# Optimization experiments

Measured on AMD Instinct MI355X. Metric: run time of the kernel, lower is better.

Reference implementation:

```python
import jax, jax.numpy as jnp
import numpy as np

B, L, D = 8, 2048, 512
H, P = 8, 4
C = D // H  # dim_per_head


def setup_inputs() -> dict:
    key = jax.random.key(0)
    ks = jax.random.split(key, 11)
    sc = lambda k, shape, s=0.02: jax.random.normal(k, shape, jnp.float32) * s
    return dict(
        query=jax.random.normal(ks[0], (B, L, D), jnp.float32),
        key_in=jax.random.normal(ks[1], (B, L, D), jnp.float32),
        value=jax.random.normal(ks[2], (B, L, D), jnp.float32),
        W_v=sc(ks[3], (D, D)), b_v=jnp.zeros((D,), jnp.float32),
        W_off=sc(ks[4], (D, H * P * 2), 0.01), b_off=sc(ks[5], (H * P * 2,), 0.2),
        W_aw=sc(ks[6], (D, H * P), 0.01), b_aw=jnp.zeros((H * P,), jnp.float32),
        W_out=sc(ks[7], (D, D)), b_out=jnp.zeros((D,), jnp.float32),
    )


def reference(query, key_in, value, W_v, b_v, W_off, b_off, W_aw, b_aw, W_out, b_out):
    # value projection
    v = value @ W_v + b_v                                        # (B,L,D)
    # sampling offsets and attention weights from the query
    off = (query @ W_off + b_off).reshape(B, L, H, P, 2)         # (B,L,H,P,2)
    aw = jax.nn.softmax((query @ W_aw + b_aw).reshape(B, L, H, P), axis=-1)
    # reference point for query i is (x=linspace[0]=0, y=linspace[i]) because
    # the torch code slices reference_points[:, :, :, :1, :]
    ref_y = jnp.linspace(0.0, 1.0, L, dtype=jnp.float32)
    loc_x = jnp.clip(off[..., 0], 0.0, 1.0)                      # ref_x = 0
    loc_y = jnp.clip(off[..., 1] + ref_y[None, :, None, None], 0.0, 1.0)
    # grid_sample, align_corners=False, input (BH, C, 1, L)
    ix = ((loc_x + 1.0) * L - 1.0) * 0.5                         # width coord in [ (L-1)/2, L-0.5 ]
    iy = loc_y * 0.5                                             # ((y+1)*1 - 1)/2
    ix0 = jnp.floor(ix)
    fx = ix - ix0
    iy0 = jnp.floor(iy)
    fy = iy - iy0
    # height dim has size 1: row iy0 valid iff ==0, row iy0+1 valid iff ==0 (zero padding)
    ywt = (1.0 - fy) * (iy0 == 0.0).astype(jnp.float32) + fy * ((iy0 + 1.0) == 0.0).astype(jnp.float32)
    i0 = ix0.astype(jnp.int32)
    i1 = i0 + 1

    perm = lambda a: a.transpose(0, 2, 1, 3)                     # (B,L,H,P) -> (B,H,L,P)
    i0p, i1p = perm(i0), perm(i1)
    vh = v.reshape(B, L, H, C).transpose(0, 2, 1, 3)             # (B,H,L,C)

    gather = jax.vmap(jax.vmap(lambda vm, ii: vm[ii]))           # (L,C),(L,P) -> (L,P,C)
    m0 = ((i0p >= 0) & (i0p < L)).astype(jnp.float32)[..., None]
    m1 = ((i1p >= 0) & (i1p < L)).astype(jnp.float32)[..., None]
    g0 = gather(vh, jnp.clip(i0p, 0, L - 1)) * m0                # (B,H,L,P,C)
    g1 = gather(vh, jnp.clip(i1p, 0, L - 1)) * m1

    fxp = perm(fx)[..., None]
    ywtp = perm(ywt)[..., None]
    samp = ywtp * ((1.0 - fxp) * g0 + fxp * g1)                  # (B,H,L,P,C)
    out = (samp * perm(aw)[..., None]).sum(axis=3)               # (B,H,L,C)
    out = out.transpose(0, 2, 1, 3).reshape(B, L, D)
    return out @ W_out + b_out
```

## Files before the change

### kernel.cpp

```cpp
#include <hip/hip_runtime.h>
#include <stdint.h>

#define M_ROWS 16384
#define PSZF (16384 * 96)

using short8  = __attribute__((ext_vector_type(8))) short;
using floatx4 = __attribute__((ext_vector_type(4))) float;

__device__ __forceinline__ unsigned short f2bf(float f) {
  union { float f; unsigned u; } v; v.f = f;
  unsigned r = v.u + 0x7fffu + ((v.u >> 16) & 1u);
  return (unsigned short)(r >> 16);
}
__device__ __forceinline__ float bf2f(unsigned short u) {
  union { unsigned u; float f; } v; v.u = ((unsigned)u) << 16; return v.f;
}

__device__ __forceinline__ void load_lds16(const unsigned short* g, unsigned short* l) {
  __builtin_amdgcn_global_load_lds(
      (const __attribute__((address_space(1))) unsigned int*)g,
      (__attribute__((address_space(3))) unsigned int*)l, 16, 0, 0);
}

__device__ __forceinline__ void store_val(float* p, float v) { *p = v; }
__device__ __forceinline__ void store_val(unsigned short* p, float v) { *p = f2bf(v); }

__global__ __launch_bounds__(256) void conv_all(const float* __restrict__ value,
                                                const float* __restrict__ query,
                                                unsigned short* __restrict__ val_bf,
                                                unsigned short* __restrict__ Qhi,
                                                unsigned short* __restrict__ Qlo) {
  int i = blockIdx.x * 256 + threadIdx.x;
  if (i < 2097152) {
    float4 v = ((const float4*)value)[i];
    ushort4 o;
    o.x = f2bf(v.x); o.y = f2bf(v.y); o.z = f2bf(v.z); o.w = f2bf(v.w);
    ((ushort4*)val_bf)[i] = o;
  } else {
    int j = i - 2097152;
    float4 v = ((const float4*)query)[j];
    ushort4 hi, lo;
    hi.x = f2bf(v.x); hi.y = f2bf(v.y); hi.z = f2bf(v.z); hi.w = f2bf(v.w);
    lo.x = f2bf(v.x - bf2f(hi.x)); lo.y = f2bf(v.y - bf2f(hi.y));
    lo.z = f2bf(v.z - bf2f(hi.z)); lo.w = f2bf(v.w - bf2f(hi.w));
    ((ushort4*)Qhi)[j] = hi;
    ((ushort4*)Qlo)[j] = lo;
  }
}

__global__ __launch_bounds__(256) void prep_w(const float* __restrict__ W_v,
                                              const float* __restrict__ W_out,
                                              const float* __restrict__ Woff,
                                              const float* __restrict__ Waw,
                                              const float* __restrict__ boff,
                                              const float* __restrict__ baw,
                                              unsigned short* __restrict__ Wv_t,
                                              unsigned short* __restrict__ Wo_t,
                                              unsigned short* __restrict__ Bhi,
                                              unsigned short* __restrict__ Blo,
                                              float* __restrict__ bcat) {
  int idx = blockIdx.x * 256 + threadIdx.x;
  if (idx < 262144) {
    int n = idx >> 9, k = idx & 511;
    Wv_t[idx] = f2bf(W_v[(k << 9) + n]);
  } else if (idx < 524288) {
    int t = idx - 262144;
    int n = t >> 9, k = t & 511;
    Wo_t[t] = f2bf(W_out[(k << 9) + n]);
  } else if (idx < 524288 + 49152) {
    int t = idx - 524288;
    int n = t >> 9, k = t & 511;
    float w = (n < 64) ? Woff[(k << 6) + n] : Waw[(k << 5) + (n - 64)];
    unsigned short hi = f2bf(w);
    Bhi[t] = hi;
    Blo[t] = f2bf(w - bf2f(hi));
  } else if (idx < 524288 + 49152 + 96) {
    int t = idx - 524288 - 49152;
    bcat[t] = (t < 64) ? boff[t] : baw[t - 64];
  }
}

template <typename OutT>
__global__ __launch_bounds__(256) void gemm_bt(const unsigned short* __restrict__ A,
                                               const unsigned short* __restrict__ Bt,
                                               const float* __restrict__ bias,
                                               OutT* __restrict__ C, int N, int K) {
  __shared__ __align__(16) unsigned short lA[128 * 32];
  __shared__ __align__(16) unsigned short lB[128 * 32];
  int tid  = threadIdx.x;
  int lane = tid & 63, wv = tid >> 6;
  int wm = wv & 1, wn = wv >> 1;
  int lrow = lane & 15, quad = lane >> 4;
  int rowBlk = blockIdx.y * 128, colBlk = blockIdx.x * 128;

  const unsigned short* Ab = A + (size_t)rowBlk * K;
  const unsigned short* Bb = Bt + (size_t)colBlk * K;
  int r0 = tid >> 2;
  int c0 = (tid & 3) << 3;

  floatx4 acc[4][4];
#pragma unroll
  for (int i = 0; i < 4; i++)
#pragma unroll
    for (int j = 0; j < 4; j++) acc[i][j] = (floatx4){0.f, 0.f, 0.f, 0.f};

  for (int k0 = 0; k0 < K; k0 += 32) {
    load_lds16(Ab + (size_t)r0 * K + k0 + c0,        lA + tid * 8);
    load_lds16(Ab + (size_t)(r0 + 64) * K + k0 + c0, lA + 2048 + tid * 8);
    load_lds16(Bb + (size_t)r0 * K + k0 + c0,        lB + tid * 8);
    load_lds16(Bb + (size_t)(r0 + 64) * K + k0 + c0, lB + 2048 + tid * 8);
    __syncthreads();

    short8 a[4], b[4];
#pragma unroll
    for (int mi = 0; mi < 4; mi++)
      a[mi] = *(const short8*)&lA[(wm * 64 + mi * 16 + lrow) * 32 + quad * 8];
#pragma unroll
    for (int ni = 0; ni < 4; ni++)
      b[ni] = *(const short8*)&lB[(wn * 64 + ni * 16 + lrow) * 32 + quad * 8];
#pragma unroll
    for (int mi = 0; mi < 4; mi++)
#pragma unroll
      for (int ni = 0; ni < 4; ni++)
        acc[mi][ni] = __builtin_amdgcn_mfma_f32_16x16x32_bf16(a[mi], b[ni], acc[mi][ni], 0, 0, 0);
    __syncthreads();
  }

#pragma unroll
  for (int ni = 0; ni < 4; ni++) {
    int col = colBlk + wn * 64 + ni * 16 + lrow;
    float bv = bias[col];
#pragma unroll
    for (int mi = 0; mi < 4; mi++) {
      int row = rowBlk + wm * 64 + mi * 16 + quad * 4;
#pragma unroll
      for (int r = 0; r < 4; r++)
        store_val(&C[(size_t)(row + r) * N + col], acc[mi][ni][r] + bv);
    }
  }
}

__global__ __launch_bounds__(256) void offaw2(const unsigned short* __restrict__ Qhi,
                                              const unsigned short* __restrict__ Qlo,
                                              const unsigned short* __restrict__ Bhi,
                                              const unsigned short* __restrict__ Blo,
                                              const float* __restrict__ bcat,
                                              float* __restrict__ P) {
  __shared__ __align__(16) unsigned short lAhi[64 * 32];
  __shared__ __align__(16) unsigned short lAlo[64 * 32];
  __shared__ __align__(16) unsigned short lBhi[96 * 32];
  __shared__ __align__(16) unsigned short lBlo[96 * 32];
  int khalf = blockIdx.x;
  int row0 = blockIdx.y * 64;
  int tid = threadIdx.x;
  int lane = tid & 63, wv = tid >> 6;
  int wm = wv & 1, wn = wv >> 1;
  int lrow = lane & 15, quad = lane >> 4;
  int kbase = khalf << 8;

  int an = tid >> 2, ac = (tid & 3) << 3;
  const unsigned short* qhb = Qhi + (size_t)(row0 + an) * 512 + kbase + ac;
  const unsigned short* qlb = Qlo + (size_t)(row0 + an) * 512 + kbase + ac;
  int bn = tid >> 2, bc = (tid & 3) << 3;
  int e2 = 256 + tid;
  int bn2 = e2 >> 2, bc2 = (e2 & 3) << 3;

  floatx4 acc[2][3];
#pragma unroll
  for (int i = 0; i < 2; i++)
#pragma unroll
    for (int j = 0; j < 3; j++) acc[i][j] = (floatx4){0.f, 0.f, 0.f, 0.f};

  for (int k0 = 0; k0 < 256; k0 += 32) {
    load_lds16(qhb + k0, lAhi + tid * 8);
    load_lds16(qlb + k0, lAlo + tid * 8);
    load_lds16(Bhi + (size_t)bn * 512 + kbase + k0 + bc, lBhi + tid * 8);
    load_lds16(Blo + (size_t)bn * 512 + kbase + k0 + bc, lBlo + tid * 8);
    if (tid < 128) {
      load_lds16(Bhi + (size_t)bn2 * 512 + kbase + k0 + bc2, lBhi + e2 * 8);
      load_lds16(Blo + (size_t)bn2 * 512 + kbase + k0 + bc2, lBlo + e2 * 8);
    }
    __syncthreads();

    short8 ah[2], al[2], bh[3], bl[3];
#pragma unroll
    for (int mi = 0; mi < 2; mi++) {
      int r = (wm * 32 + mi * 16 + lrow) * 32 + quad * 8;
      ah[mi] = *(const short8*)&lAhi[r];
      al[mi] = *(const short8*)&lAlo[r];
    }
#pragma unroll
    for (int ni = 0; ni < 3; ni++) {
      int r = (wn * 48 + ni * 16 + lrow) * 32 + quad * 8;
      bh[ni] = *(const short8*)&lBhi[r];
      bl[ni] = *(const short8*)&lBlo[r];
    }
#pragma unroll
    for (int mi = 0; mi < 2; mi++)
#pragma unroll
      for (int ni = 0; ni < 3; ni++) {
        acc[mi][ni] = __builtin_amdgcn_mfma_f32_16x16x32_bf16(ah[mi], bh[ni], acc[mi][ni], 0, 0, 0);
        acc[mi][ni] = __builtin_amdgcn_mfma_f32_16x16x32_bf16(ah[mi], bl[ni], acc[mi][ni], 0, 0, 0);
        acc[mi][ni] = __builtin_amdgcn_mfma_f32_16x16x32_bf16(al[mi], bh[ni], acc[mi][ni], 0, 0, 0);
      }
    __syncthreads();
  }

  float* out = P + (size_t)khalf * PSZF;
#pragma unroll
  for (int ni = 0; ni < 3; ni++) {
    int col = wn * 48 + ni * 16 + lrow;
    float bv = (khalf == 0) ? bcat[col] : 0.0f;
#pragma unroll
    for (int mi = 0; mi < 2; mi++) {
      int row = row0 + wm * 32 + mi * 16 + quad * 4;
#pragma unroll
      for (int r = 0; r < 4; r++)
        out[(size_t)(row + r) * 96 + col] = acc[mi][ni][r] + bv;
    }
  }
}

__global__ __launch_bounds__(256) void sample_kernel(const float* __restrict__ P,
                                                     const unsigned short* __restrict__ v,
                                                     unsigned short* __restrict__ attn) {
  int row = blockIdx.x;
  int b = row >> 11, l = row & 2047;
  __shared__ float s_w0[32], s_w1[32];
  __shared__ int s_i0[32], s_i1[32];
  int tid = threadIdx.x;

  if (tid < 32) {
    int base = row * 96;
    float lg = P[base + 64 + tid] + P[PSZF + base + 64 + tid];
    float mx = fmaxf(lg, __shfl_xor(lg, 1));
    mx = fmaxf(mx, __shfl_xor(mx, 2));
    float e = __expf(lg - mx);
    float s = e + __shfl_xor(e, 1);
    s = s + __shfl_xor(s, 2);
    float aw = e / s;

    float ox = P[base + 2 * tid] + P[PSZF + base + 2 * tid];
    float oy = P[base + 2 * tid + 1] + P[PSZF + base + 2 * tid + 1];
    float refy = (float)l * (1.0f / 2047.0f);
    float lx = fminf(fmaxf(ox, 0.0f), 1.0f);
    float ly = fminf(fmaxf(oy + refy, 0.0f), 1.0f);
    float ix = ((lx + 1.0f) * 2048.0f - 1.0f) * 0.5f;
    float ywt = 1.0f - ly * 0.5f;
    float ix0 = floorf(ix);
    float fx = ix - ix0;
    int i0 = (int)ix0;
    int i1 = i0 + 1;
    s_w0[tid] = aw * ywt * (1.0f - fx);
    s_w1[tid] = (i1 < 2048) ? (aw * ywt * fx) : 0.0f;
    s_i0[tid] = i0;
    s_i1[tid] = (i1 < 2048) ? i1 : 2047;
  }
  __syncthreads();

  const unsigned short* vb = v + ((size_t)(b << 11)) * 512;
  int h = tid >> 5, c = (tid & 31) << 1;
  const unsigned short* vhc = vb + h * 64 + c;
  float ax = 0.0f, ay = 0.0f;
#pragma unroll
  for (int p = 0; p < 4; p++) {
    int t = (h << 2) + p;
    unsigned g0 = *(const unsigned*)(vhc + ((size_t)s_i0[t] << 9));
    unsigned g1 = *(const unsigned*)(vhc + ((size_t)s_i1[t] << 9));
    float w0 = s_w0[t], w1 = s_w1[t];
    ax += w0 * bf2f((unsigned short)g0) + w1 * bf2f((unsigned short)g1);
    ay += w0 * bf2f((unsigned short)(g0 >> 16)) + w1 * bf2f((unsigned short)(g1 >> 16));
  }
  unsigned packed = (unsigned)f2bf(ax) | ((unsigned)f2bf(ay) << 16);
  *(unsigned*)(attn + (size_t)row * 512 + h * 64 + c) = packed;
}

extern "C" void kernel_launch(void* const* d_in, const int* in_sizes, int n_in,
                              void* d_out, int out_size, void* d_ws, size_t ws_size,
                              hipStream_t stream) {
  (void)in_sizes; (void)n_in; (void)out_size; (void)ws_size;
  const float* query = (const float*)d_in[0];
  const float* value = (const float*)d_in[2];
  const float* W_v   = (const float*)d_in[3];
  const float* b_v   = (const float*)d_in[4];
  const float* W_off = (const float*)d_in[5];
  const float* b_off = (const float*)d_in[6];
  const float* W_aw  = (const float*)d_in[7];
  const float* b_aw  = (const float*)d_in[8];
  const float* W_out = (const float*)d_in[9];
  const float* b_out = (const float*)d_in[10];
  float* out = (float*)d_out;

  char* ws = (char*)d_ws;
  const size_t MB = 1ull << 20;
  unsigned short* val_bf = (unsigned short*)(ws);
  unsigned short* attn   = val_bf;
  unsigned short* v_bf   = (unsigned short*)(ws + 16 * MB);
  unsigned short* Qhi    = (unsigned short*)(ws + 32 * MB);
  unsigned short* Qlo    = (unsigned short*)(ws + 48 * MB);
  float* offP            = (float*)(ws + 64 * MB);
  unsigned short* Wv_t   = (unsigned short*)(ws + 80 * MB);
  unsigned short* Wo_t   = (unsigned short*)(ws + 80 * MB + 524288);
  unsigned short* Bhi    = (unsigned short*)(ws + 81 * MB);
  unsigned short* Blo    = (unsigned short*)(ws + 81 * MB + 98304);
  float* bcat            = (float*)(ws + 81 * MB + 196608);

  conv_all<<<16384, 256, 0, stream>>>(value, query, val_bf, Qhi, Qlo);
  prep_w<<<2241, 256, 0, stream>>>(W_v, W_out, W_off, W_aw, b_off, b_aw,
                                   Wv_t, Wo_t, Bhi, Blo, bcat);

  gemm_bt<unsigned short><<<dim3(4, 128), 256, 0, stream>>>(val_bf, Wv_t, b_v, v_bf, 512, 512);
  offaw2<<<dim3(2, 256), 256, 0, stream>>>(Qhi, Qlo, Bhi, Blo, bcat, offP);
  sample_kernel<<<16384, 256, 0, stream>>>(offP, v_bf, attn);
  gemm_bt<float><<<dim3(4, 128), 256, 0, stream>>>(attn, Wo_t, b_out, out, 512, 512);
}
```

Baseline: 217.9 us.

## Fuse query bf16 split into offset GEMM and merge prep and GEMM launches

The query hi/lo bf16 split now happens inside the offset/attention-weight GEMM, which reads fp32 query directly and writes the pieces to LDS. This removes the Qhi/Qlo intermediate buffers and their global round trip. The value conversion and the weight prep are merged into one kernel, and the value-projection GEMM and the offset GEMM run as one launch with a split block range, cutting launch count and letting the two GEMMs overlap. The trade-off is more VALU work and plain (non-async) stores to LDS in the offset kernel, plus a mixed-workload kernel whose shared-memory size is set by the larger branch.

```diff
diff --git a/kernel.cpp b/kernel.cpp
--- a/kernel.cpp
+++ b/kernel.cpp
@@ -1,7 +1,6 @@
 #include <hip/hip_runtime.h>
 #include <stdint.h>
 
-#define M_ROWS 16384
 #define PSZF (16384 * 96)
 
 using short8  = __attribute__((ext_vector_type(8))) short;
@@ -16,7 +15,7 @@
   union { unsigned u; float f; } v; v.u = ((unsigned)u) << 16; return v.f;
 }
 
-__device__ __forceinline__ void load_lds16(const unsigned short* g, unsigned short* l) {
+__device__ __forceinline__ void load_lds16(const void* g, void* l) {
   __builtin_amdgcn_global_load_lds(
       (const __attribute__((address_space(1))) unsigned int*)g,
       (__attribute__((address_space(3))) unsigned int*)l, 16, 0, 0);
@@ -25,73 +24,66 @@
 __device__ __forceinline__ void store_val(float* p, float v) { *p = v; }
 __device__ __forceinline__ void store_val(unsigned short* p, float v) { *p = f2bf(v); }
 
-__global__ __launch_bounds__(256) void conv_all(const float* __restrict__ value,
-                                                const float* __restrict__ query,
+__global__ __launch_bounds__(256) void prep_all(const float* __restrict__ value,
+                                                const float* __restrict__ W_v,
+                                                const float* __restrict__ W_out,
+                                                const float* __restrict__ Woff,
+                                                const float* __restrict__ Waw,
+                                                const float* __restrict__ boff,
+                                                const float* __restrict__ baw,
                                                 unsigned short* __restrict__ val_bf,
-                                                unsigned short* __restrict__ Qhi,
-                                                unsigned short* __restrict__ Qlo) {
-  int i = blockIdx.x * 256 + threadIdx.x;
-  if (i < 2097152) {
-    float4 v = ((const float4*)value)[i];
+                                                unsigned short* __restrict__ Wv_t,
+                                                unsigned short* __restrict__ Wo_t,
+                                                unsigned short* __restrict__ Bhi,
+                                                unsigned short* __restrict__ Blo,
+                                                float* __restrict__ bcat) {
+  int idx = blockIdx.x * 256 + threadIdx.x;
+  if (idx < 2097152) {
+    float4 v = ((const float4*)value)[idx];
     ushort4 o;
     o.x = f2bf(v.x); o.y = f2bf(v.y); o.z = f2bf(v.z); o.w = f2bf(v.w);
-    ((ushort4*)val_bf)[i] = o;
-  } else {
-    int j = i - 2097152;
-    float4 v = ((const float4*)query)[j];
-    ushort4 hi, lo;
-    hi.x = f2bf(v.x); hi.y = f2bf(v.y); hi.z = f2bf(v.z); hi.w = f2bf(v.w);
-    lo.x = f2bf(v.x - bf2f(hi.x)); lo.y = f2bf(v.y - bf2f(hi.y));
-    lo.z = f2bf(v.z - bf2f(hi.z)); lo.w = f2bf(v.w - bf2f(hi.w));
-    ((ushort4*)Qhi)[j] = hi;
-    ((ushort4*)Qlo)[j] = lo;
-  }
-}
-
-__global__ __launch_bounds__(256) void prep_w(const float* __restrict__ W_v,
-                                              const float* __restrict__ W_out,
-                                              const float* __restrict__ Woff,
-                                              const float* __restrict__ Waw,
-                                              const float* __restrict__ boff,
-                                              const float* __restrict__ baw,
-                                              unsigned short* __restrict__ Wv_t,
-                                              unsigned short* __restrict__ Wo_t,
-                                              unsigned short* __restrict__ Bhi,
-                                              unsigned short* __restrict__ Blo,
-                                              float* __restrict__ bcat) {
-  int idx = blockIdx.x * 256 + threadIdx.x;
-  if (idx < 262144) {
-    int n = idx >> 9, k = idx & 511;
-    Wv_t[idx] = f2bf(W_v[(k << 9) + n]);
-  } else if (idx < 524288) {
-    int t = idx - 262144;
+    ((ushort4*)val_bf)[idx] = o;
+    return;
+  }
+  int t = idx - 2097152;
+  if (t < 262144) {
+    int n = t >> 9, k = t & 511;
+    Wv_t[t] = f2bf(W_v[(k << 9) + n]);
+    return;
+  }
+  t -= 262144;
+  if (t < 262144) {
     int n = t >> 9, k = t & 511;
     Wo_t[t] = f2bf(W_out[(k << 9) + n]);
-  } else if (idx < 524288 + 49152) {
-    int t = idx - 524288;
+    return;
+  }
+  t -= 262144;
+  if (t < 49152) {
     int n = t >> 9, k = t & 511;
     float w = (n < 64) ? Woff[(k << 6) + n] : Waw[(k << 5) + (n - 64)];
     unsigned short hi = f2bf(w);
     Bhi[t] = hi;
     Blo[t] = f2bf(w - bf2f(hi));
-  } else if (idx < 524288 + 49152 + 96) {
-    int t = idx - 524288 - 49152;
-    bcat[t] = (t < 64) ? boff[t] : baw[t - 64];
-  }
+    return;
+  }
+  t -= 49152;
+  if (t < 96) bcat[t] = (t < 64) ? boff[t] : baw[t - 64];
 }
 
 template <typename OutT>
-__global__ __launch_bounds__(256) void gemm_bt(const unsigned short* __restrict__ A,
-                                               const unsigned short* __restrict__ Bt,
-                                               const float* __restrict__ bias,
-                                               OutT* __restrict__ C, int N, int K) {
-  __shared__ __align__(16) unsigned short lA[128 * 32];
-  __shared__ __align__(16) unsigned short lB[128 * 32];
+__device__ __forceinline__ void gemm_body(unsigned char* smem,
+                                          const unsigned short* __restrict__ A,
+                                          const unsigned short* __restrict__ Bt,
+                                          const float* __restrict__ bias,
+                                          OutT* __restrict__ C, int N, int K,
+                                          int bx, int by) {
+  unsigned short* lA = (unsigned short*)smem;
+  unsigned short* lB = (unsigned short*)(smem + 8192);
   int tid  = threadIdx.x;
   int lane = tid & 63, wv = tid >> 6;
   int wm = wv & 1, wn = wv >> 1;
   int lrow = lane & 15, quad = lane >> 4;
-  int rowBlk = blockIdx.y * 128, colBlk = blockIdx.x * 128;
+  int rowBlk = by * 128, colBlk = bx * 128;
 
   const unsigned short* Ab = A + (size_t)rowBlk * K;
   const unsigned short* Bb = Bt + (size_t)colBlk * K;
@@ -140,30 +132,22 @@
   }
 }
 
-__global__ __launch_bounds__(256) void offaw2(const unsigned short* __restrict__ Qhi,
-                                              const unsigned short* __restrict__ Qlo,
-                                              const unsigned short* __restrict__ Bhi,
-                                              const unsigned short* __restrict__ Blo,
-                                              const float* __restrict__ bcat,
-                                              float* __restrict__ P) {
-  __shared__ __align__(16) unsigned short lAhi[64 * 32];
-  __shared__ __align__(16) unsigned short lAlo[64 * 32];
-  __shared__ __align__(16) unsigned short lBhi[96 * 32];
-  __shared__ __align__(16) unsigned short lBlo[96 * 32];
-  int khalf = blockIdx.x;
-  int row0 = blockIdx.y * 64;
-  int tid = threadIdx.x;
-  int lane = tid & 63, wv = tid >> 6;
-  int wm = wv & 1, wn = wv >> 1;
-  int lrow = lane & 15, quad = lane >> 4;
-  int kbase = khalf << 8;
-
-  int an = tid >> 2, ac = (tid & 3) << 3;
-  const unsigned short* qhb = Qhi + (size_t)(row0 + an) * 512 + kbase + ac;
-  const unsigned short* qlb = Qlo + (size_t)(row0 + an) * 512 + kbase + ac;
-  int bn = tid >> 2, bc = (tid & 3) << 3;
-  int e2 = 256 + tid;
-  int bn2 = e2 >> 2, bc2 = (e2 & 3) << 3;
+__device__ __forceinline__ void offaw_body(unsigned char* smem,
+                                           const float* __restrict__ Q,
+                                           const unsigned short* __restrict__ Bhi,
+                                           const unsigned short* __restrict__ Blo,
+                                           const float* __restrict__ bcat,
+                                           float* __restrict__ P, int bid) {
+  unsigned short* lAhi = (unsigned short*)smem;
+  unsigned short* lAlo = (unsigned short*)(smem + 4096);
+  unsigned short* lBhi = (unsigned short*)(smem + 8192);
+  unsigned short* lBlo = (unsigned short*)(smem + 14336);
+  int khalf = bid >> 8, row0 = (bid & 255) * 64, kbase = khalf << 8;
+  int tid = threadIdx.x, lane = tid & 63, wv = tid >> 6;
+  int wm = wv & 1, wn = wv >> 1, lrow = lane & 15, quad = lane >> 4;
+
+  int ar = tid >> 2, ac = (tid & 3) << 3;
+  const float* qp = Q + (size_t)(row0 + ar) * 512 + kbase + ac;
 
   floatx4 acc[2][3];
 #pragma unroll
@@ -172,13 +156,29 @@
     for (int j = 0; j < 3; j++) acc[i][j] = (floatx4){0.f, 0.f, 0.f, 0.f};
 
   for (int k0 = 0; k0 < 256; k0 += 32) {
-    load_lds16(qhb + k0, lAhi + tid * 8);
-    load_lds16(qlb + k0, lAlo + tid * 8);
-    load_lds16(Bhi + (size_t)bn * 512 + kbase + k0 + bc, lBhi + tid * 8);
-    load_lds16(Blo + (size_t)bn * 512 + kbase + k0 + bc, lBlo + tid * 8);
-    if (tid < 128) {
-      load_lds16(Bhi + (size_t)bn2 * 512 + kbase + k0 + bc2, lBhi + e2 * 8);
-      load_lds16(Blo + (size_t)bn2 * 512 + kbase + k0 + bc2, lBlo + e2 * 8);
+    float4 v0 = *(const float4*)(qp + k0);
+    float4 v1 = *(const float4*)(qp + k0 + 4);
+    float vv[8] = {v0.x, v0.y, v0.z, v0.w, v1.x, v1.y, v1.z, v1.w};
+    short8 h8, l8;
+#pragma unroll
+    for (int e = 0; e < 8; e++) {
+      union { float f; unsigned u; } t; t.f = vv[e];
+      unsigned r = t.u + 0x7fffu + ((t.u >> 16) & 1u);
+      h8[e] = (short)(r >> 16);
+      union { unsigned u; float f; } hf; hf.u = r & 0xffff0000u;
+      union { float f; unsigned u; } rb; rb.f = vv[e] - hf.f;
+      l8[e] = (short)(rb.u >> 16);
+    }
+    *(short8*)&lAhi[tid * 8] = h8;
+    *(short8*)&lAlo[tid * 8] = l8;
+#pragma unroll
+    for (int j = 0; j < 3; j++) {
+      int widx = wv + (j << 2);
+      const unsigned short* src = (widx < 6) ? Bhi : Blo;
+      unsigned short* dst = (widx < 6) ? lBhi : lBlo;
+      int c = (((widx < 6) ? widx : widx - 6) << 6) + lane;
+      int n = c >> 2, cc = (c & 3) << 3;
+      load_lds16(src + (size_t)n * 512 + kbase + k0 + cc, dst + c * 8);
     }
     __syncthreads();
 
@@ -219,6 +219,31 @@
         out[(size_t)(row + r) * 96 + col] = acc[mi][ni][r] + bv;
     }
   }
+}
+
+__global__ __launch_bounds__(256) void mega_k2(const unsigned short* __restrict__ val_bf,
+                                               const unsigned short* __restrict__ Wv_t,
+                                               const float* __restrict__ b_v,
+                                               unsigned short* __restrict__ v_bf,
+                                               const float* __restrict__ query,
+                                               const unsigned short* __restrict__ Bhi,
+                                               const unsigned short* __restrict__ Blo,
+                                               const float* __restrict__ bcat,
+                                               float* __restrict__ offP) {
+  __shared__ __align__(16) unsigned char smem[20480];
+  int bx = blockIdx.x;
+  if (bx < 512)
+    gemm_body<unsigned short>(smem, val_bf, Wv_t, b_v, v_bf, 512, 512, bx & 3, bx >> 2);
+  else
+    offaw_body(smem, query, Bhi, Blo, bcat, offP, bx - 512);
+}
+
+__global__ __launch_bounds__(256) void gemm2_k(const unsigned short* __restrict__ A,
+                                               const unsigned short* __restrict__ Bt,
+                                               const float* __restrict__ bias,
+                                               float* __restrict__ C) {
+  __shared__ __align__(16) unsigned char smem[16384];
+  gemm_body<float>(smem, A, Bt, bias, C, 512, 512, blockIdx.x & 3, blockIdx.x >> 2);
 }
 
 __global__ __launch_bounds__(256) void sample_kernel(const float* __restrict__ P,
@@ -296,21 +321,16 @@
   unsigned short* val_bf = (unsigned short*)(ws);
   unsigned short* attn   = val_bf;
   unsigned short* v_bf   = (unsigned short*)(ws + 16 * MB);
-  unsigned short* Qhi    = (unsigned short*)(ws + 32 * MB);
-  unsigned short* Qlo    = (unsigned short*)(ws + 48 * MB);
-  float* offP            = (float*)(ws + 64 * MB);
-  unsigned short* Wv_t   = (unsigned short*)(ws + 80 * MB);
-  unsigned short* Wo_t   = (unsigned short*)(ws + 80 * MB + 524288);
-  unsigned short* Bhi    = (unsigned short*)(ws + 81 * MB);
-  unsigned short* Blo    = (unsigned short*)(ws + 81 * MB + 98304);
-  float* bcat            = (float*)(ws + 81 * MB + 196608);
-
-  conv_all<<<16384, 256, 0, stream>>>(value, query, val_bf, Qhi, Qlo);
-  prep_w<<<2241, 256, 0, stream>>>(W_v, W_out, W_off, W_aw, b_off, b_aw,
-                                   Wv_t, Wo_t, Bhi, Blo, bcat);
-
-  gemm_bt<unsigned short><<<dim3(4, 128), 256, 0, stream>>>(val_bf, Wv_t, b_v, v_bf, 512, 512);
-  offaw2<<<dim3(2, 256), 256, 0, stream>>>(Qhi, Qlo, Bhi, Blo, bcat, offP);
+  float* offP            = (float*)(ws + 32 * MB);
+  unsigned short* Wv_t   = (unsigned short*)(ws + 48 * MB);
+  unsigned short* Wo_t   = (unsigned short*)(ws + 48 * MB + 524288);
+  unsigned short* Bhi    = (unsigned short*)(ws + 49 * MB);
+  unsigned short* Blo    = (unsigned short*)(ws + 49 * MB + 98304);
+  float* bcat            = (float*)(ws + 49 * MB + 196608);
+
+  prep_all<<<10433, 256, 0, stream>>>(value, W_v, W_out, W_off, W_aw, b_off, b_aw,
+                                      val_bf, Wv_t, Wo_t, Bhi, Blo, bcat);
+  mega_k2<<<1024, 256, 0, stream>>>(val_bf, Wv_t, b_v, v_bf, query, Bhi, Blo, bcat, offP);
   sample_kernel<<<16384, 256, 0, stream>>>(offP, v_bf, attn);
-  gemm_bt<float><<<dim3(4, 128), 256, 0, stream>>>(attn, Wo_t, b_out, out, 512, 512);
-}
+  gemm2_k<<<512, 256, 0, stream>>>(attn, Wo_t, b_out, out);
+}
```

Result: faster. 206.8 us (-5.1%).
